# Kernel tuning notes

Hardware: AMD Instinct MI355X
Metric: run time of the kernel (lower is better)

Reference implementation:

```python
import jax, jax.numpy as jnp
import numpy as np
import math

B, N, DIM, H, DH = 2, 2048, 768, 12, 64
NUM_BUCKETS, MAX_DIST = 32, 128


def _rel_pos_bucket(n):
    # causal bucketing as in T5RelativePositionBias._relative_position_bucket
    rel = jnp.arange(n)[None, :] - jnp.arange(n)[:, None]          # k_pos - q_pos
    neg = jnp.maximum(-rel, 0)                                     # n = max(-rel, 0)
    max_exact = NUM_BUCKETS // 2
    is_small = neg < max_exact
    val_large = max_exact + (
        jnp.log(jnp.maximum(neg, 1).astype(jnp.float32) / max_exact)
        / math.log(MAX_DIST / max_exact) * (NUM_BUCKETS - max_exact)
    ).astype(jnp.int32)
    val_large = jnp.minimum(val_large, NUM_BUCKETS - 1)
    return jnp.where(is_small, neg, val_large)                     # [n, n] int32


def setup_inputs() -> dict:
    key = jax.random.key(0)
    ks = jax.random.split(key, 6)
    s = DIM ** -0.5
    x = jax.random.normal(ks[0], (B, N, DIM), jnp.float32)
    mask = jnp.ones((B, N), dtype=bool)
    Wq = jax.random.normal(ks[1], (DIM, H * DH), jnp.float32) * s
    Wk = jax.random.normal(ks[2], (DIM, H * DH), jnp.float32) * s
    Wv = jax.random.normal(ks[3], (DIM, H * DH), jnp.float32) * s
    Wo = jax.random.normal(ks[4], (H * DH, DIM), jnp.float32) * s
    rel_emb = jax.random.normal(ks[5], (NUM_BUCKETS, H), jnp.float32) * 0.02
    return {"x": x, "mask": mask, "Wq": Wq, "Wk": Wk, "Wv": Wv, "Wo": Wo, "rel_emb": rel_emb}


def reference(x, mask, Wq, Wk, Wv, Wo, rel_emb):
    b, n, _ = x.shape
    scale = DH ** -0.5
    # projections -> [b, h, n, d]
    q = (x @ Wq).reshape(b, n, H, DH).transpose(0, 2, 1, 3) * scale
    k = (x @ Wk).reshape(b, n, H, DH).transpose(0, 2, 1, 3)
    v = (x @ Wv).reshape(b, n, H, DH).transpose(0, 2, 1, 3)
    sim = jnp.einsum('bhid,bhjd->bhij', q, k)                      # [b, h, n, n]
    # relative position bias, also scaled by dim_head**-0.5
    bias = rel_emb[_rel_pos_bucket(n)]                             # [n, n, h]
    sim = sim + jnp.transpose(bias, (2, 0, 1))[None] * scale
    mask_value = -jnp.finfo(sim.dtype).max
    # key/query padding mask: ~mask[:, None, :, None] masks rows (query dim)
    sim = jnp.where(mask[:, None, :, None], sim, mask_value)
    causal = jnp.triu(jnp.ones((n, n), dtype=bool), 1)
    sim = jnp.where(causal[None, None], mask_value, sim)
    attn = jax.nn.softmax(sim, axis=-1)
    out = jnp.einsum('bhij,bhjd->bhid', attn, v)                   # [b, h, n, d]
    out = out.transpose(0, 2, 1, 3).reshape(b, n, H * DH)
    return out @ Wo
```

## Files before the change

### kernel.cpp

```cpp
#include <hip/hip_runtime.h>
#include <math.h>

#define NSEQ 2048
#define HDIM 768
#define NHEAD 12
#define DHEAD 64
#define CHUNK 6
#define NJOBS 51
#define EXP_C1 1.44269504f
#define EXP_C0 -17.3123405f

typedef __attribute__((ext_vector_type(8))) short short8;
typedef __attribute__((ext_vector_type(4))) float f32x4;

static __device__ __forceinline__ unsigned short f2bf(float x) {
    unsigned int u = __float_as_uint(x);
    unsigned int r = (u + 0x7fffu + ((u >> 16) & 1u)) >> 16;
    return (unsigned short)r;
}
static __device__ __forceinline__ float bf2f(unsigned short u) {
    return __uint_as_float(((unsigned int)u) << 16);
}

#define GLD_LDS16(g, l)                                                  \
    __builtin_amdgcn_global_load_lds(                                    \
        (const __attribute__((address_space(1))) void*)(g),              \
        (__attribute__((address_space(3))) void*)(l), 16, 0, 0)

__global__ __launch_bounds__(256) void prep(const float* __restrict__ X,
                                            const float* __restrict__ Wq,
                                            const float* __restrict__ Wk,
                                            const float* __restrict__ Wv,
                                            const float* __restrict__ Wo,
                                            const float* __restrict__ relemb,
                                            unsigned short* __restrict__ Xb,
                                            unsigned short* __restrict__ Wt,
                                            unsigned short* __restrict__ rbg) {
    __shared__ float tb[64][65];
    const int z = blockIdx.x;
    if (z < 576) {
        const int wsel = z / 144, tt = z % 144;
        const int n0 = (tt % 12) * 64, k0 = (tt / 12) * 64;
        const float* W = (wsel == 0) ? Wq : (wsel == 1) ? Wk : (wsel == 2) ? Wv : Wo;
        const float scale = (wsel == 0) ? 0.125f : 1.0f;
        unsigned short* dst = Wt + (size_t)wsel * HDIM * HDIM;
        const int r = threadIdx.x >> 4;
        const int c4 = (threadIdx.x & 15) * 4;
#pragma unroll
        for (int i = 0; i < 4; i++) {
            int row = i * 16 + r;
            float4 v = *(const float4*)(W + (size_t)(k0 + row) * HDIM + n0 + c4);
            tb[c4 + 0][row] = v.x * scale;
            tb[c4 + 1][row] = v.y * scale;
            tb[c4 + 2][row] = v.z * scale;
            tb[c4 + 3][row] = v.w * scale;
        }
        __syncthreads();
#pragma unroll
        for (int i = 0; i < 4; i++) {
            int row = i * 16 + r;
            ushort4 o;
            o.x = f2bf(tb[row][c4 + 0]);
            o.y = f2bf(tb[row][c4 + 1]);
            o.z = f2bf(tb[row][c4 + 2]);
            o.w = f2bf(tb[row][c4 + 3]);
            *(ushort4*)(dst + (size_t)(n0 + row) * HDIM + k0 + c4) = o;
        }
    } else if (z < 960) {
        int base = (z - 576) * 2048 + threadIdx.x;
#pragma unroll
        for (int u = 0; u < 8; u++) {
            int f = base + u * 256;
            float4 v = ((const float4*)X)[f];
            ushort4 o;
            o.x = f2bf(v.x); o.y = f2bf(v.y); o.z = f2bf(v.z); o.w = f2bf(v.w);
            ((ushort4*)Xb)[f] = o;
        }
    } else {
        int idx = (z - 960) * 256 + threadIdx.x;
        int h = idx >> 11;
        int d = idx & (NSEQ - 1);
        int bucket;
        if (d < 16) {
            bucket = d;
        } else {
            float v = logf((float)d * (1.0f / 16.0f)) * (16.0f / logf(8.0f));
            bucket = 16 + (int)v;
            if (bucket > 31) bucket = 31;
        }
        rbg[h * NSEQ + d] = f2bf(relemb[bucket * NHEAD + h] * 0.125f);
    }
}

template <int MODE, int MT>
__global__ __launch_bounds__(256) void gemm_bt(const unsigned short* __restrict__ A,
                                               const unsigned short* __restrict__ Bt,
                                               void* __restrict__ Cout) {
    __shared__ unsigned short As[(MT * 32) * 32];
    __shared__ unsigned short Bs[128 * 32];

    const int tid = threadIdx.x;
    const int w = tid >> 6, lane = tid & 63;
    const int ln = lane & 15, qd = lane >> 4;
    const int wm = w >> 1, wn = w & 1;
    const int mat = blockIdx.x / (HDIM / 128);
    const int n0 = (blockIdx.x % (HDIM / 128)) * 128;
    const int m0 = blockIdx.y * (MT * 32);
    const unsigned short* Bm = Bt + (size_t)mat * HDIM * HDIM;

    const int scol = (lane & 3) * 8;
    const int arow = w * (MT * 8) + (lane >> 2);
    const int brow = w * 32 + (lane >> 2);
    const unsigned short* agp = A + (size_t)(m0 + arow) * HDIM + scol;
    const unsigned short* bgp = Bm + (size_t)(n0 + brow) * HDIM + scol;
    unsigned short* al = As + (w * (MT * 8)) * 32;
    unsigned short* bl = Bs + (w * 32) * 32;

    f32x4 acc[MT][4];
#pragma unroll
    for (int i = 0; i < MT; i++)
#pragma unroll
        for (int j = 0; j < 4; j++) acc[i][j] = (f32x4){0.f, 0.f, 0.f, 0.f};

    for (int k0 = 0; k0 < HDIM; k0 += 32) {
        __syncthreads();
        GLD_LDS16(agp + k0, al);
        if (MT == 4) GLD_LDS16(agp + 16 * HDIM + k0, al + 16 * 32);
        GLD_LDS16(bgp + k0, bl);
        GLD_LDS16(bgp + 16 * HDIM + k0, bl + 16 * 32);
        __syncthreads();

        short8 af[MT], bf[4];
#pragma unroll
        for (int mt = 0; mt < MT; mt++)
            af[mt] = *(const short8*)&As[(wm * (MT * 16) + mt * 16 + ln) * 32 + qd * 8];
#pragma unroll
        for (int nt = 0; nt < 4; nt++)
            bf[nt] = *(const short8*)&Bs[(wn * 64 + nt * 16 + ln) * 32 + qd * 8];
#pragma unroll
        for (int mt = 0; mt < MT; mt++)
#pragma unroll
            for (int nt = 0; nt < 4; nt++)
                acc[mt][nt] = __builtin_amdgcn_mfma_f32_16x16x32_bf16(
                    af[mt], bf[nt], acc[mt][nt], 0, 0, 0);
    }

    if constexpr (MODE == 0) {
        float* C = (float*)Cout;
#pragma unroll
        for (int mt = 0; mt < MT; mt++)
#pragma unroll
            for (int r = 0; r < 4; r++) {
                int m = m0 + wm * (MT * 16) + mt * 16 + qd * 4 + r;
#pragma unroll
                for (int nt = 0; nt < 4; nt++) {
                    int n = n0 + wn * 64 + nt * 16 + ln;
                    C[(size_t)m * HDIM + n] = acc[mt][nt][r];
                }
            }
    } else {
        const size_t QKVE = (size_t)2 * NHEAD * NSEQ * DHEAD;
        unsigned short* dstm = (unsigned short*)Cout + (size_t)mat * QKVE;
#pragma unroll
        for (int mt = 0; mt < MT; mt++)
#pragma unroll
            for (int r = 0; r < 4; r++) {
                int m = m0 + wm * (MT * 16) + mt * 16 + qd * 4 + r;
                int b = m >> 11, tok = m & (NSEQ - 1);
#pragma unroll
                for (int nt = 0; nt < 4; nt++) {
                    int col = n0 + wn * 64 + nt * 16 + ln;
                    int h = col >> 6, dh = col & 63;
                    dstm[((size_t)(b * NHEAD + h) * NSEQ + tok) * DHEAD + dh] =
                        f2bf(acc[mt][nt][r]);
                }
            }
    }
}

__global__ __launch_bounds__(256) void vtrans(const unsigned short* __restrict__ Vn,
                                              unsigned short* __restrict__ Vt) {
    __shared__ unsigned short Ls[64 * 66];
    const int tid = threadIdx.x;
    const int tok0 = blockIdx.x * 64;
    const size_t bh = blockIdx.y;
    const unsigned short* src = Vn + (bh * NSEQ + tok0) * DHEAD;
    unsigned short* dst = Vt + bh * DHEAD * NSEQ + tok0;

    const int rr = tid >> 3, cc = (tid & 7) * 8;
#pragma unroll
    for (int u = 0; u < 2; u++)
        *(short8*)&Ls[(u * 32 + rr) * 66 + cc] =
            *(const short8*)(src + (size_t)(u * 32 + rr) * DHEAD + cc);
    __syncthreads();
#pragma unroll
    for (int u = 0; u < 2; u++) {
        int dhr = u * 32 + rr;
        short8 v;
#pragma unroll
        for (int e = 0; e < 8; e++) v[e] = Ls[(cc + e) * 66 + dhr];
        *(short8*)(dst + (size_t)dhr * NSEQ + cc) = v;
    }
}

__global__ __launch_bounds__(256) void attn_mfma(const unsigned short* __restrict__ Q,
                                                 const unsigned short* __restrict__ K,
                                                 const unsigned short* __restrict__ Vt_g,
                                                 const unsigned short* __restrict__ rbg,
                                                 unsigned short* __restrict__ AO,
                                                 unsigned short* __restrict__ Of,
                                                 float* __restrict__ Pl) {
    __shared__ __align__(16) unsigned short Ks[64 * 72];
    __shared__ __align__(16) unsigned short Vt[64 * 72];
    __shared__ __align__(16) unsigned short Ps[4 * 32 * 72];
    __shared__ __align__(16) unsigned short rbs[512];

    const int tid = threadIdx.x;
    const int w = tid >> 6;
    const int lane = tid & 63;
    const int ln = lane & 15;
    const int qd = lane >> 4;
    const int job = blockIdx.x;
    const int h = blockIdx.y;
    const int b = blockIdx.z;

    int qt = 0, cb = 0;
    for (;;) {
        int c = (2 * qt + 2 + CHUNK - 1) / CHUNK;
        if (job < cb + c) break;
        cb += c;
        qt++;
    }
    const int c = (2 * qt + 2 + CHUNK - 1) / CHUNK;
    const int jd = job - cb;
    const int ntk = 2 * qt + 2;
    const int t0 = ntk * jd / c, t1 = ntk * (jd + 1) / c;
    const int i0 = qt * 128;

    const int bhl = b * NHEAD + h;
    const size_t bh = (size_t)bhl;
    const unsigned short* Kb = K + bh * NSEQ * DHEAD;
    const unsigned short* Vg = Vt_g + bh * DHEAD * NSEQ;

    const int wbase = i0 - t1 * 64 + 1;
    const unsigned short NEG = f2bf(-1e30f);
#pragma unroll
    for (int u = 0; u < 2; u++) {
        int idx = u * 256 + tid;
        int d = wbase + idx;
        int dc = d < 0 ? 0 : (d > NSEQ - 1 ? NSEQ - 1 : d);
        rbs[idx] = (d < 0) ? NEG : rbg[h * NSEQ + dc];
    }

    short8 qf[2][2];
#pragma unroll
    for (int rg = 0; rg < 2; rg++) {
        const unsigned short* qrow =
            Q + (bh * NSEQ + i0 + w * 32 + rg * 16 + ln) * DHEAD;
        qf[rg][0] = *(const short8*)(qrow + qd * 8);
        qf[rg][1] = *(const short8*)(qrow + 32 + qd * 8);
    }

    short8 ones;
#pragma unroll
    for (int e = 0; e < 8; e++) ones[e] = (short)0x3F80;

    f32x4 o[2][4];
#pragma unroll
    for (int rg = 0; rg < 2; rg++)
#pragma unroll
        for (int cc = 0; cc < 4; cc++) o[rg][cc] = (f32x4){0.f, 0.f, 0.f, 0.f};
    f32x4 o4[2] = {{0.f, 0.f, 0.f, 0.f}, {0.f, 0.f, 0.f, 0.f}};

    int bqw[2];
#pragma unroll
    for (int rg = 0; rg < 2; rg++)
        bqw[rg] = i0 + w * 32 + rg * 16 + qd * 4 - ln - wbase;

    unsigned short* Pw = Ps + w * 32 * 72;

    const int sr = tid >> 3;
    const int sc = (tid & 7) * 8;
    short8 kp[2], vp[2];
    {
        const int jb = t0 * 64;
#pragma unroll
        for (int u = 0; u < 2; u++) {
            kp[u] = *(const short8*)(Kb + (size_t)(jb + u * 32 + sr) * DHEAD + sc);
            vp[u] = *(const short8*)(Vg + (size_t)(u * 32 + sr) * NSEQ + jb + sc);
        }
    }

    for (int t = t0; t < t1; t++) {
        const int jt = t * 64;
        __syncthreads();
#pragma unroll
        for (int u = 0; u < 2; u++) {
            *(short8*)&Ks[(u * 32 + sr) * 72 + sc] = kp[u];
            *(short8*)&Vt[(u * 32 + sr) * 72 + sc] = vp[u];
        }
        __syncthreads();
        if (t + 1 < t1) {
            const int jn = jt + 64;
#pragma unroll
            for (int u = 0; u < 2; u++) {
                kp[u] = *(const short8*)(Kb + (size_t)(jn + u * 32 + sr) * DHEAD + sc);
                vp[u] = *(const short8*)(Vg + (size_t)(u * 32 + sr) * NSEQ + jn + sc);
            }
        }

        short8 kf[4][2];
#pragma unroll
        for (int cc = 0; cc < 4; cc++) {
            kf[cc][0] = *(const short8*)&Ks[(cc * 16 + ln) * 72 + qd * 8];
            kf[cc][1] = *(const short8*)&Ks[(cc * 16 + ln) * 72 + 32 + qd * 8];
        }

#pragma unroll
        for (int rg = 0; rg < 2; rg++) {
            f32x4 s[4] = {{0.f, 0.f, 0.f, 0.f}, {0.f, 0.f, 0.f, 0.f},
                          {0.f, 0.f, 0.f, 0.f}, {0.f, 0.f, 0.f, 0.f}};
#pragma unroll
            for (int cc = 0; cc < 4; cc++) {
                s[cc] = __builtin_amdgcn_mfma_f32_16x16x32_bf16(qf[rg][0], kf[cc][0],
                                                               s[cc], 0, 0, 0);
                s[cc] = __builtin_amdgcn_mfma_f32_16x16x32_bf16(qf[rg][1], kf[cc][1],
                                                               s[cc], 0, 0, 0);
            }
#pragma unroll
            for (int cc = 0; cc < 4; cc++) {
                const int ib = bqw[rg] - jt - cc * 16;
#pragma unroll
                for (int r = 0; r < 4; r++) {
                    float sv = s[cc][r] + bf2f(rbs[ib + r]);
                    float p = __builtin_amdgcn_exp2f(__fmaf_rn(sv, EXP_C1, EXP_C0));
                    Pw[(rg * 16 + qd * 4 + r) * 72 + cc * 16 + ln] = f2bf(p);
                }
            }
        }

        short8 vf[4][2];
#pragma unroll
        for (int cc = 0; cc < 4; cc++) {
            vf[cc][0] = *(const short8*)&Vt[(cc * 16 + ln) * 72 + qd * 8];
            vf[cc][1] = *(const short8*)&Vt[(cc * 16 + ln) * 72 + 32 + qd * 8];
        }

#pragma unroll
        for (int rg = 0; rg < 2; rg++) {
            short8 pa0 = *(const short8*)(Pw + (rg * 16 + ln) * 72 + qd * 8);
            short8 pa1 = *(const short8*)(Pw + (rg * 16 + ln) * 72 + 32 + qd * 8);
#pragma unroll
            for (int cc = 0; cc < 4; cc++) {
                o[rg][cc] = __builtin_amdgcn_mfma_f32_16x16x32_bf16(pa0, vf[cc][0],
                                                                    o[rg][cc], 0, 0, 0);
                o[rg][cc] = __builtin_amdgcn_mfma_f32_16x16x32_bf16(pa1, vf[cc][1],
                                                                    o[rg][cc], 0, 0, 0);
            }
            o4[rg] = __builtin_amdgcn_mfma_f32_16x16x32_bf16(pa0, ones, o4[rg], 0, 0, 0);
            o4[rg] = __builtin_amdgcn_mfma_f32_16x16x32_bf16(pa1, ones, o4[rg], 0, 0, 0);
        }
    }

    if (job < 3) {
#pragma unroll
        for (int rg = 0; rg < 2; rg++) {
            unsigned short* aop = AO +
                ((size_t)(b * NSEQ) + i0 + w * 32 + rg * 16 + qd * 4) * HDIM +
                h * DHEAD + ln;
#pragma unroll
            for (int r = 0; r < 4; r++) {
                float inv = 1.0f / o4[rg][r];
#pragma unroll
                for (int cc = 0; cc < 4; cc++)
                    aop[(size_t)r * HDIM + cc * 16] = f2bf(o[rg][cc][r] * inv);
            }
        }
    } else {
        const size_t gc = (size_t)bhl * NJOBS + job;
#pragma unroll
        for (int rg = 0; rg < 2; rg++) {
            const int rowl = w * 32 + rg * 16 + qd * 4;
            unsigned short* po = Of + (gc * 128 + rowl) * 64 + ln;
#pragma unroll
            for (int r = 0; r < 4; r++) {
                float inv = 1.0f / o4[rg][r];
#pragma unroll
                for (int cc = 0; cc < 4; cc++)
                    po[(size_t)r * 64 + cc * 16] = f2bf(o[rg][cc][r] * inv);
            }
            if (ln == 0) {
#pragma unroll
                for (int r = 0; r < 4; r++) Pl[gc * 128 + rowl + r] = o4[rg][r];
            }
        }
    }
}

__global__ __launch_bounds__(256) void attn_merge(const unsigned short* __restrict__ Of,
                                                  const float* __restrict__ Pl,
                                                  unsigned short* __restrict__ AO) {
    const int tid = threadIdx.x;
    const int row_g = blockIdx.x * 4 + (tid >> 6);
    const int dh = tid & 63;
    const int bhl = row_g / (NSEQ - 384);
    const int tok = 384 + row_g % (NSEQ - 384);
    const int b = bhl / NHEAD, h = bhl % NHEAD;
    const int g2 = tok >> 7;

    int cb = 0;
    for (int qq = 0; qq < g2; qq++) cb += (2 * qq + 2 + CHUNK - 1) / CHUNK;
    const int c = (2 * g2 + 2 + CHUNK - 1) / CHUNK;
    const int rowl = tok & 127;

    float acc = 0.f, W = 0.f;
    for (int i = 0; i < c; i++) {
        size_t gc = (size_t)bhl * NJOBS + cb + i;
        float l = Pl[gc * 128 + rowl];
        acc += l * bf2f(Of[(gc * 128 + rowl) * 64 + dh]);
        W += l;
    }
    AO[((size_t)(b * NSEQ) + tok) * HDIM + h * DHEAD + dh] = f2bf(acc / W);
}

extern "C" void kernel_launch(void* const* d_in, const int* in_sizes, int n_in,
                              void* d_out, int out_size, void* d_ws, size_t ws_size,
                              hipStream_t stream) {
    const float* x      = (const float*)d_in[0];
    const float* Wq     = (const float*)d_in[2];
    const float* Wk     = (const float*)d_in[3];
    const float* Wv     = (const float*)d_in[4];
    const float* Wo     = (const float*)d_in[5];
    const float* relemb = (const float*)d_in[6];
    float* out = (float*)d_out;

    const size_t QKV = (size_t)2 * NHEAD * NSEQ * DHEAD;
    const size_t NCHUNK = (size_t)24 * NJOBS;
    unsigned short* q   = (unsigned short*)d_ws;
    unsigned short* k   = q + QKV;
    unsigned short* v   = k + QKV;
    unsigned short* vT  = v + QKV;
    unsigned short* aob = vT + QKV;
    unsigned short* xb  = aob + QKV;
    unsigned short* wt  = xb + QKV;
    unsigned short* rbg = wt + (size_t)4 * HDIM * HDIM;
    unsigned short* Of  = rbg + (size_t)NHEAD * NSEQ;
    float* Pl = (float*)(Of + NCHUNK * 128 * 64);

    prep<<<1056, 256, 0, stream>>>(x, Wq, Wk, Wv, Wo, relemb, xb, wt, rbg);

    gemm_bt<1, 4><<<dim3(3 * HDIM / 128, (2 * NSEQ) / 128), 256, 0, stream>>>(
        xb, wt, q);

    vtrans<<<dim3(NSEQ / 64, 2 * NHEAD), 256, 0, stream>>>(v, vT);

    attn_mfma<<<dim3(NJOBS, NHEAD, 2), 256, 0, stream>>>(q, k, vT, rbg, aob, Of, Pl);

    attn_merge<<<(24 * (NSEQ - 384)) / 4, 256, 0, stream>>>(Of, Pl, aob);

    gemm_bt<0, 2><<<dim3(HDIM / 128, (2 * NSEQ) / 64), 256, 0, stream>>>(
        aob, wt + (size_t)3 * HDIM * HDIM, out);
}
```

Baseline: 180.7 us.

## Load K/V fragments directly from global, drop LDS staging, remap grid per XCD

Removes the shared-memory staging of K and V tiles and their two per-iteration barriers. Each wave now loads its MFMA fragments straight from global memory and relies on the cache for reuse across waves. The grid is flattened to 1D and remapped so that each XCD handles three (batch, head) pairs, which keeps a head's K/V in that XCD's L2. Launch bounds now request 4 blocks per CU. The cost is redundant global and L2 traffic, since all four waves reload the same K/V, and the software prefetch that overlapped loads with compute is gone.

```diff
diff --git a/kernel.cpp b/kernel.cpp
--- a/kernel.cpp
+++ b/kernel.cpp
@@ -203,15 +203,13 @@
     }
 }
 
-__global__ __launch_bounds__(256) void attn_mfma(const unsigned short* __restrict__ Q,
-                                                 const unsigned short* __restrict__ K,
-                                                 const unsigned short* __restrict__ Vt_g,
-                                                 const unsigned short* __restrict__ rbg,
-                                                 unsigned short* __restrict__ AO,
-                                                 unsigned short* __restrict__ Of,
-                                                 float* __restrict__ Pl) {
-    __shared__ __align__(16) unsigned short Ks[64 * 72];
-    __shared__ __align__(16) unsigned short Vt[64 * 72];
+__global__ __launch_bounds__(256, 4) void attn_mfma(const unsigned short* __restrict__ Q,
+                                                    const unsigned short* __restrict__ K,
+                                                    const unsigned short* __restrict__ Vt_g,
+                                                    const unsigned short* __restrict__ rbg,
+                                                    unsigned short* __restrict__ AO,
+                                                    unsigned short* __restrict__ Of,
+                                                    float* __restrict__ Pl) {
     __shared__ __align__(16) unsigned short Ps[4 * 32 * 72];
     __shared__ __align__(16) unsigned short rbs[512];
 
@@ -220,9 +218,14 @@
     const int lane = tid & 63;
     const int ln = lane & 15;
     const int qd = lane >> 4;
-    const int job = blockIdx.x;
-    const int h = blockIdx.y;
-    const int b = blockIdx.z;
+
+    const int bid = blockIdx.x;
+    const int xcd = bid & 7;
+    const int slot = bid >> 3;
+    const int bhl = xcd * 3 + slot / NJOBS;
+    const int job = slot % NJOBS;
+    const int b = bhl / NHEAD;
+    const int h = bhl - b * NHEAD;
 
     int qt = 0, cb = 0;
     for (;;) {
@@ -237,7 +240,6 @@
     const int t0 = ntk * jd / c, t1 = ntk * (jd + 1) / c;
     const int i0 = qt * 128;
 
-    const int bhl = b * NHEAD + h;
     const size_t bh = (size_t)bhl;
     const unsigned short* Kb = K + bh * NSEQ * DHEAD;
     const unsigned short* Vg = Vt_g + bh * DHEAD * NSEQ;
@@ -261,6 +263,8 @@
         qf[rg][1] = *(const short8*)(qrow + 32 + qd * 8);
     }
 
+    __syncthreads();
+
     short8 ones;
 #pragma unroll
     for (int e = 0; e < 8; e++) ones[e] = (short)0x3F80;
@@ -279,41 +283,16 @@
 
     unsigned short* Pw = Ps + w * 32 * 72;
 
-    const int sr = tid >> 3;
-    const int sc = (tid & 7) * 8;
-    short8 kp[2], vp[2];
-    {
-        const int jb = t0 * 64;
-#pragma unroll
-        for (int u = 0; u < 2; u++) {
-            kp[u] = *(const short8*)(Kb + (size_t)(jb + u * 32 + sr) * DHEAD + sc);
-            vp[u] = *(const short8*)(Vg + (size_t)(u * 32 + sr) * NSEQ + jb + sc);
-        }
-    }
-
     for (int t = t0; t < t1; t++) {
         const int jt = t * 64;
-        __syncthreads();
-#pragma unroll
-        for (int u = 0; u < 2; u++) {
-            *(short8*)&Ks[(u * 32 + sr) * 72 + sc] = kp[u];
-            *(short8*)&Vt[(u * 32 + sr) * 72 + sc] = vp[u];
-        }
-        __syncthreads();
-        if (t + 1 < t1) {
-            const int jn = jt + 64;
-#pragma unroll
-            for (int u = 0; u < 2; u++) {
-                kp[u] = *(const short8*)(Kb + (size_t)(jn + u * 32 + sr) * DHEAD + sc);
-                vp[u] = *(const short8*)(Vg + (size_t)(u * 32 + sr) * NSEQ + jn + sc);
-            }
-        }
 
         short8 kf[4][2];
 #pragma unroll
         for (int cc = 0; cc < 4; cc++) {
-            kf[cc][0] = *(const short8*)&Ks[(cc * 16 + ln) * 72 + qd * 8];
-            kf[cc][1] = *(const short8*)&Ks[(cc * 16 + ln) * 72 + 32 + qd * 8];
+            const unsigned short* kr =
+                Kb + (size_t)(jt + cc * 16 + ln) * DHEAD + qd * 8;
+            kf[cc][0] = *(const short8*)kr;
+            kf[cc][1] = *(const short8*)(kr + 32);
         }
 
 #pragma unroll
@@ -342,8 +321,10 @@
         short8 vf[4][2];
 #pragma unroll
         for (int cc = 0; cc < 4; cc++) {
-            vf[cc][0] = *(const short8*)&Vt[(cc * 16 + ln) * 72 + qd * 8];
-            vf[cc][1] = *(const short8*)&Vt[(cc * 16 + ln) * 72 + 32 + qd * 8];
+            const unsigned short* vr =
+                Vg + (size_t)(cc * 16 + ln) * NSEQ + jt + qd * 8;
+            vf[cc][0] = *(const short8*)vr;
+            vf[cc][1] = *(const short8*)(vr + 32);
         }
 
 #pragma unroll
@@ -454,7 +435,7 @@
 
     vtrans<<<dim3(NSEQ / 64, 2 * NHEAD), 256, 0, stream>>>(v, vT);
 
-    attn_mfma<<<dim3(NJOBS, NHEAD, 2), 256, 0, stream>>>(q, k, vT, rbg, aob, Of, Pl);
+    attn_mfma<<<dim3(8 * 3 * NJOBS), 256, 0, stream>>>(q, k, vT, rbg, aob, Of, Pl);
 
     attn_merge<<<(24 * (NSEQ - 384)) / 4, 256, 0, stream>>>(Of, Pl, aob);
 
```

Result: slower. 209.0 us (+15.7%).
